# Kernel tuning notes

Measured on AMD Instinct MI355X. Metric: run time of the kernel, lower is better.

The kernel has to match this reference:

```python
import jax, jax.numpy as jnp
import numpy as np

GRID = 3
K = GRID ** 3          # keypoints per proposal (grid rep)
RADIUS = 0.2
NSAMPLE = 16


def _rotz(t):
    c, s = jnp.cos(t), jnp.sin(t)
    z, o = jnp.zeros_like(t), jnp.ones_like(t)
    return jnp.stack([jnp.stack([c, -s, z], -1),
                      jnp.stack([s,  c, z], -1),
                      jnp.stack([z,  z, o], -1)], -2)  # [..., 3, 3]


def _grid_keypoints(boxes, origins, heading):
    # boxes: [B,P,6] = (left,back,down,right,front,up) absolute distances from origin
    B, P, _ = boxes.shape
    ii = jnp.stack(jnp.meshgrid(jnp.arange(GRID), jnp.arange(GRID), jnp.arange(GRID), indexing='ij'), -1)
    dense = ii.reshape(K, 3).astype(boxes.dtype)  # same order as ones(g,g,g).nonzero()
    size = boxes[..., 0:3] + boxes[..., 3:6]                       # [B,P,3]
    local = (dense + 0.5) / GRID * size[:, :, None, :] - boxes[..., None, 0:3]  # [B,P,K,3]
    R = _rotz(heading)                                             # [B,P,3,3]
    pts = jnp.einsum('bpkc,bpcd->bpkd', local, R) + origins[:, :, None, :]
    return pts.reshape(B, P * K, 3)


def _ball_query(key_pts, seed_xyz):
    # key_pts [B,M,3], seed_xyz [B,N,3] -> neighbor indices [B,M,NSAMPLE]
    N = seed_xyz.shape[1]
    d2 = (jnp.sum(key_pts ** 2, -1)[:, :, None]
          + jnp.sum(seed_xyz ** 2, -1)[:, None, :]
          - 2.0 * jnp.einsum('bmc,bnc->bmn', key_pts, seed_xyz))   # [B,M,N]
    cand = jnp.where(d2 < RADIUS ** 2, jnp.arange(N, dtype=jnp.int32), N)
    idx = -jax.lax.top_k(-cand, NSAMPLE)[0]  # first NSAMPLE in-radius indices, ascending
    first = idx[..., 0:1]
    fill = jnp.where(first == N, 0, first)   # empty ball -> index 0 (CUDA kernel default)
    return jnp.where(idx == N, fill, idx)


def _forward(seed_xyz, seed_features, boxes, origins, heading, W1, b1, W2, b2, W3, b3, Wr, br):
    B, P = boxes.shape[:2]
    key_pts = _grid_keypoints(boxes, origins, heading)             # [B,M,3], M=P*K
    idx = _ball_query(key_pts, seed_xyz)                           # [B,M,S]
    b_idx = jnp.arange(B)[:, None, None]
    gx = seed_xyz[b_idx, idx]                                      # [B,M,S,3]
    gf = jnp.transpose(seed_features, (0, 2, 1))[b_idx, idx]       # [B,M,S,C]
    gxyz = (gx - key_pts[:, :, None, :]) / RADIUS                  # normalize_xyz=True
    x = jnp.concatenate([gxyz, gf], -1)                            # use_xyz: [B,M,S,3+C]
    x = jax.nn.relu(x @ W1 + b1)                                   # shared per-point MLP
    x = jax.nn.relu(x @ W2 + b2)
    x = jax.nn.relu(x @ W3 + b3)
    x = jnp.max(x, axis=2)                                         # max-pool over ball -> [B,M,32]
    f = x.reshape(B, P, K, 32)
    # original: [B,32,M] -> view(B,32,P,K) -> transpose(2,3) -> reshape(B,32*K,P)
    f = jnp.transpose(f, (0, 1, 3, 2)).reshape(B, P, 32 * K)       # channel-major (c*K+k) layout
    out = f @ Wr.T + br                                            # 1x1 conv reduce -> [B,P,128]
    return jnp.transpose(out, (0, 2, 1))                           # [B,128,P]


def setup_inputs() -> dict:
    key = jax.random.key(0)
    ks = jax.random.split(key, 9)
    B, N, C, P = 2, 1024, 256, 256
    return {
        'seed_xyz': jax.random.normal(ks[0], (B, N, 3), jnp.float32),
        'seed_features': jax.random.normal(ks[1], (B, C, N), jnp.float32),
        'boxes': jax.random.uniform(ks[2], (B, P, 6), jnp.float32, 0.1, 1.0),
        'origins': jax.random.normal(ks[3], (B, P, 3), jnp.float32),
        'heading': jax.random.uniform(ks[4], (B, P), jnp.float32, 0.0, 6.2831853),
        'W1': jax.random.normal(ks[5], (C + 3, 128), jnp.float32) * 0.05,
        'b1': jnp.zeros((128,), jnp.float32),
        'W2': jax.random.normal(ks[6], (128, 64), jnp.float32) * 0.05,
        'b2': jnp.zeros((64,), jnp.float32),
        'W3': jax.random.normal(ks[7], (64, 32), jnp.float32) * 0.05,
        'b3': jnp.zeros((32,), jnp.float32),
        'Wr': jax.random.normal(ks[8], (128, 32 * K), jnp.float32) * 0.05,
        'br': jnp.zeros((128,), jnp.float32),
    }


def reference(seed_xyz, seed_features, boxes, origins, heading, W1, b1, W2, b2, W3, b3, Wr, br):
    return _forward(seed_xyz, seed_features, boxes, origins, heading, W1, b1, W2, b2, W3, b3, Wr, br)
```

## Files before the change

kernel.cpp:

```cpp
#include <hip/hip_runtime.h>

#define B_ 2
#define N_ 1024
#define C_ 256
#define P_ 256
#define K_ 27
#define M_ (P_ * K_)
#define TOTKP (B_ * M_)
#define NS 16
#define R2C 0.04f
#define QDIM 864


#define PREP_FPRE0   0
#define PREP_WRT0    256
#define PREP_OINIT0  364
#define PREP_BALLQ0  620
#define PREP_NBLK    4076

__global__ __launch_bounds__(256) void prep_k(
    const float* __restrict__ sf, const float* __restrict__ W1,
    const float* __restrict__ b1, const float* __restrict__ Wr,
    const float* __restrict__ br, const float* __restrict__ seed_xyz,
    const float* __restrict__ boxes, const float* __restrict__ origins,
    const float* __restrict__ heading,
    float* __restrict__ F, float* __restrict__ WrT, float* __restrict__ out,
    float4* __restrict__ kp4, int* __restrict__ cntw, int* __restrict__ idxw)
{
    __shared__ __align__(16) float ssf[C_ * 8];
    int tid = threadIdx.x;
    int bid = blockIdx.x;

    if (bid < PREP_WRT0) {
        int b = bid >> 7;
        int n0 = (bid & 127) * 8;
        for (int e = tid; e < C_ * 8; e += 256) {
            int c = e >> 3, i = e & 7;
            ssf[e] = sf[(b * C_ + c) * N_ + n0 + i];
        }
        __syncthreads();
        int j = tid & 127;
        int h = tid >> 7;
        float acc[4];
        float bj = b1[j];
#pragma unroll
        for (int i = 0; i < 4; i++) acc[i] = bj;
#pragma unroll 8
        for (int c = 0; c < C_; ++c) {
            float w = W1[(3 + c) * 128 + j];
            float4 s = *(const float4*)&ssf[c * 8 + h * 4];
            acc[0] = fmaf(s.x, w, acc[0]);
            acc[1] = fmaf(s.y, w, acc[1]);
            acc[2] = fmaf(s.z, w, acc[2]);
            acc[3] = fmaf(s.w, w, acc[3]);
        }
#pragma unroll
        for (int i = 0; i < 4; i++)
            F[(b * N_ + n0 + h * 4 + i) * 128 + j] = acc[i];
    } else if (bid < PREP_OINIT0) {
        int e4 = (bid - PREP_WRT0) * 256 + tid;
        int j = e4 / 216, qq = e4 - j * 216;
        float4 v = ((const float4*)(Wr + j * QDIM))[qq];
        int q0 = qq * 4;
        WrT[(q0 + 0) * 128 + j] = v.x;
        WrT[(q0 + 1) * 128 + j] = v.y;
        WrT[(q0 + 2) * 128 + j] = v.z;
        WrT[(q0 + 3) * 128 + j] = v.w;
    } else if (bid < PREP_BALLQ0) {
        int id = (bid - PREP_OINIT0) * 256 + tid;
        out[id] = br[(id >> 8) & 127];
    } else {
        int wid = tid >> 6, lane = tid & 63;
        int kpg = (bid - PREP_BALLQ0) * 4 + wid;
        int b = kpg / M_;
        int m = kpg - b * M_;
        int p = m / K_, a = m - p * K_;

        const float* bx = boxes + (b * P_ + p) * 6;
        const float* og = origins + (b * P_ + p) * 3;
        float th = heading[b * P_ + p];
        float di = (float)(a / 9), dj = (float)((a / 3) % 3), dk = (float)(a % 3);
        float s0 = __fadd_rn(bx[0], bx[3]);
        float s1 = __fadd_rn(bx[1], bx[4]);
        float s2 = __fadd_rn(bx[2], bx[5]);
        float lx = __fsub_rn(__fmul_rn(__fdiv_rn(__fadd_rn(di, 0.5f), 3.0f), s0), bx[0]);
        float ly = __fsub_rn(__fmul_rn(__fdiv_rn(__fadd_rn(dj, 0.5f), 3.0f), s1), bx[1]);
        float lz = __fsub_rn(__fmul_rn(__fdiv_rn(__fadd_rn(dk, 0.5f), 3.0f), s2), bx[2]);
        float ct = cosf(th), st = sinf(th);
        float kx = __fadd_rn(__fadd_rn(__fmul_rn(lx, ct), __fmul_rn(ly, st)), og[0]);
        float ky = __fadd_rn(__fadd_rn(__fmul_rn(lx, -st), __fmul_rn(ly, ct)), og[1]);
        float kz = __fadd_rn(lz, og[2]);
        if (lane == 0) kp4[kpg] = make_float4(kx, ky, kz, 0.f);
        float kk = __fadd_rn(__fadd_rn(__fmul_rn(kx, kx), __fmul_rn(ky, ky)),
                             __fmul_rn(kz, kz));

        const float* sb = seed_xyz + b * (N_ * 3) + lane * 48;
        float f[48];
#pragma unroll
        for (int q = 0; q < 12; q++)
            ((float4*)f)[q] = ((const float4*)sb)[q];

        unsigned mask = 0;
#pragma unroll
        for (int i = 0; i < 16; i++) {
            float x = f[3 * i], y = f[3 * i + 1], z = f[3 * i + 2];
            float ss = __fadd_rn(__fadd_rn(__fmul_rn(x, x), __fmul_rn(y, y)),
                                 __fmul_rn(z, z));
            float dot = __fadd_rn(__fadd_rn(__fmul_rn(kx, x), __fmul_rn(ky, y)),
                                  __fmul_rn(kz, z));
            float d2 = __fsub_rn(__fadd_rn(kk, ss), __fmul_rn(2.0f, dot));
            mask |= (d2 < R2C ? 1u : 0u) << i;
        }

        int pc = __popc(mask);
        int incl = pc;
#pragma unroll
        for (int d = 1; d < 64; d <<= 1) {
            int v = __shfl_up(incl, d);
            if (lane >= d) incl += v;
        }
        int total = __shfl(incl, 63);
        int base = incl - pc;

        int* ip = idxw + kpg * NS;
        unsigned mm = mask;
        while (mm && base < NS) {
            int i = __ffs(mm) - 1;
            mm &= mm - 1;
            ip[base++] = lane * 16 + i;
        }
        if (lane == 0) cntw[kpg] = total < NS ? total : NS;
    }
}

struct Ctx {
    const float* seed; const float* F;
    const float* sW2; const float* sW3;
    float* sH1; float* sH2;
    const int* ip;
    float4 kp;
    float w1x0, w1y0, w1z0, w1x1, w1y1, w1z1, b2j, b3t;
    int lane, t, jh, b, cnt, n0;
};

template <int GS>
static __device__ __forceinline__ void do_group(const Ctx& c, int s0, float& pool)
{
    float gx[GS], gy[GS], gz[GS];
    int nn[GS];
#pragma unroll
    for (int u = 0; u < GS; u++) {
        int s = s0 + u;
        int n = (s < c.cnt) ? c.ip[s] : c.n0;
        nn[u] = n;
        const float* sp = c.seed + (c.b * N_ + n) * 3;
        gx[u] = __fdiv_rn(__fsub_rn(sp[0], c.kp.x), 0.2f);
        gy[u] = __fdiv_rn(__fsub_rn(sp[1], c.kp.y), 0.2f);
        gz[u] = __fdiv_rn(__fsub_rn(sp[2], c.kp.z), 0.2f);
    }
#pragma unroll
    for (int u = 0; u < GS; u++) {
        const float* fp = c.F + (c.b * N_ + nn[u]) * 128;
        float v0 = fp[c.lane];
        float v1 = fp[c.lane + 64];
        v0 = fmaf(gx[u], c.w1x0, fmaf(gy[u], c.w1y0, fmaf(gz[u], c.w1z0, v0)));
        v1 = fmaf(gx[u], c.w1x1, fmaf(gy[u], c.w1y1, fmaf(gz[u], c.w1z1, v1)));
        c.sH1[u * 128 + c.lane] = fmaxf(v0, 0.f);
        c.sH1[u * 128 + c.lane + 64] = fmaxf(v1, 0.f);
    }
    float acc[GS];
#pragma unroll
    for (int u = 0; u < GS; u++) acc[u] = c.b2j;
#pragma unroll
    for (int cc = 0; cc < 128; cc += 4) {
        float w0 = c.sW2[(cc + 0) * 64 + c.lane];
        float w1 = c.sW2[(cc + 1) * 64 + c.lane];
        float w2 = c.sW2[(cc + 2) * 64 + c.lane];
        float w3 = c.sW2[(cc + 3) * 64 + c.lane];
#pragma unroll
        for (int u = 0; u < GS; u++) {
            float4 h = *(const float4*)&c.sH1[u * 128 + cc];
            acc[u] = fmaf(h.x, w0, fmaf(h.y, w1, fmaf(h.z, w2, fmaf(h.w, w3, acc[u]))));
        }
    }
#pragma unroll
    for (int u = 0; u < GS; u++) c.sH2[u * 64 + c.lane] = fmaxf(acc[u], 0.f);
    float a3[GS];
#pragma unroll
    for (int u = 0; u < GS; u++) a3[u] = (c.jh == 0) ? c.b3t : 0.f;
#pragma unroll
    for (int jj = 0; jj < 32; jj += 4) {
        int j0 = c.jh * 32 + jj;
        float w0 = c.sW3[(j0 + 0) * 32 + c.t];
        float w1 = c.sW3[(j0 + 1) * 32 + c.t];
        float w2 = c.sW3[(j0 + 2) * 32 + c.t];
        float w3 = c.sW3[(j0 + 3) * 32 + c.t];
#pragma unroll
        for (int u = 0; u < GS; u++) {
            float4 h = *(const float4*)&c.sH2[u * 64 + j0];
            a3[u] = fmaf(h.x, w0, fmaf(h.y, w1, fmaf(h.z, w2, fmaf(h.w, w3, a3[u]))));
        }
    }
#pragma unroll
    for (int u = 0; u < GS; u++) {
        float v = a3[u] + __shfl_xor(a3[u], 32);
        pool = fmaxf(pool, fmaxf(v, 0.f));
    }
}

__global__ __launch_bounds__(256) void pool_k(
    const float* __restrict__ seed_xyz, const float* __restrict__ F,
    const float* __restrict__ W1, const float* __restrict__ b2g,
    const float* __restrict__ b3g, const float* __restrict__ W2g,
    const float* __restrict__ W3g, const float4* __restrict__ kp4,
    const int* __restrict__ cntw, const int* __restrict__ idxw,
    float* __restrict__ pooled)
{
    __shared__ __align__(16) float sW2[128 * 64];
    __shared__ __align__(16) float sW3[64 * 32];
    __shared__ __align__(16) float sH1[4 * 4 * 128];
    __shared__ __align__(16) float sH2[4 * 4 * 64];
    int tid = threadIdx.x;
    for (int e = tid; e < 2048; e += 256)
        ((float4*)sW2)[e] = ((const float4*)W2g)[e];
    for (int e = tid; e < 512; e += 256)
        ((float4*)sW3)[e] = ((const float4*)W3g)[e];
    __syncthreads();

    int wid = tid >> 6, lane = tid & 63;
    Ctx c;
    c.seed = seed_xyz; c.F = F;
    c.sW2 = sW2; c.sW3 = sW3;
    c.sH1 = sH1 + wid * 4 * 128;
    c.sH2 = sH2 + wid * 4 * 64;
    c.lane = lane; c.t = lane & 31; c.jh = lane >> 5;
    c.w1x0 = W1[lane];       c.w1x1 = W1[lane + 64];
    c.w1y0 = W1[128 + lane]; c.w1y1 = W1[128 + lane + 64];
    c.w1z0 = W1[256 + lane]; c.w1z1 = W1[256 + lane + 64];
    c.b2j = b2g[lane]; c.b3t = b3g[lane & 31];

    for (int i = 0; i < 2; ++i) {
        int kpg = blockIdx.x * 8 + wid * 2 + i;
        c.kp = kp4[kpg];
        c.cnt = cntw[kpg];
        c.ip = idxw + kpg * NS;
        c.b = kpg / M_;
        c.n0 = (c.cnt > 0) ? c.ip[0] : 0;
        int scnt = c.cnt < 1 ? 1 : c.cnt;
        float pool = 0.f;
        for (int s0 = 0; s0 < scnt; s0 += 4) {
            int gs = scnt - s0; gs = gs > 4 ? 4 : gs;
            switch (gs) {
                case 1: do_group<1>(c, s0, pool); break;
                case 2: do_group<2>(c, s0, pool); break;
                case 3: do_group<3>(c, s0, pool); break;
                default: do_group<4>(c, s0, pool); break;
            }
        }
        if (lane < 32) pooled[kpg * 32 + lane] = pool;
    }
}

__global__ __launch_bounds__(256) void final_k(
    const float* __restrict__ pooled, const float* __restrict__ WrT,
    float* __restrict__ out)
{
    __shared__ __align__(16) float ft[8][108];
    int tid = threadIdx.x;
    int blk = blockIdx.x;
    int c = blk & 7;
    int mt = blk >> 3;
    if (tid < 216) {
        int ri = tid / 27, k = tid - ri * 27;
        int row = mt * 8 + ri;
        int b = row >> 8, p = row & 255;
        const float* sp = pooled + ((b * M_ + p * K_) + k) * 32 + c * 4;
        float4 v = *(const float4*)sp;
        float* fp = &ft[ri][0];
        fp[k] = v.x; fp[27 + k] = v.y; fp[54 + k] = v.z; fp[81 + k] = v.w;
    }
    __syncthreads();
    int j = tid & 127;
    int rh = tid >> 7;
    float a0 = 0.f, a1 = 0.f, a2 = 0.f, a3 = 0.f;
    const float* wp = WrT + (c * 108) * 128 + j;
    const float* f0 = &ft[rh * 4 + 0][0];
    const float* f1 = &ft[rh * 4 + 1][0];
    const float* f2 = &ft[rh * 4 + 2][0];
    const float* f3 = &ft[rh * 4 + 3][0];
#pragma unroll 4
    for (int q = 0; q < 108; ++q) {
        float w = wp[q * 128];
        a0 = fmaf(f0[q], w, a0);
        a1 = fmaf(f1[q], w, a1);
        a2 = fmaf(f2[q], w, a2);
        a3 = fmaf(f3[q], w, a3);
    }
    int row0 = mt * 8 + rh * 4;
    int b0 = row0 >> 8;
    int p0 = row0 & 255;
    float* op = out + b0 * 128 * 256 + j * 256 + p0;
    atomicAdd(op + 0, a0);
    atomicAdd(op + 1, a1);
    atomicAdd(op + 2, a2);
    atomicAdd(op + 3, a3);
}

extern "C" void kernel_launch(void* const* d_in, const int* in_sizes, int n_in,
                              void* d_out, int out_size, void* d_ws, size_t ws_size,
                              hipStream_t stream)
{
    const float* seed_xyz  = (const float*)d_in[0];
    const float* seed_feat = (const float*)d_in[1];
    const float* boxes     = (const float*)d_in[2];
    const float* origins   = (const float*)d_in[3];
    const float* heading   = (const float*)d_in[4];
    const float* W1        = (const float*)d_in[5];
    const float* b1        = (const float*)d_in[6];
    const float* W2        = (const float*)d_in[7];
    const float* b2        = (const float*)d_in[8];
    const float* W3        = (const float*)d_in[9];
    const float* b3        = (const float*)d_in[10];
    const float* Wr        = (const float*)d_in[11];
    const float* br        = (const float*)d_in[12];
    float* out = (float*)d_out;

    char* ws = (char*)d_ws;
    float4* kp4    = (float4*)(ws);
    int*    cntw   = (int*)(ws + 221184);
    int*    idxw   = (int*)(ws + 276480);
    float*  F      = (float*)(ws + 1161216);
    float*  pooled = (float*)(ws + 2209792);
    float*  WrT    = (float*)(ws + 3979264);

    prep_k<<<dim3(PREP_NBLK), dim3(256), 0, stream>>>(
        seed_feat, W1, b1, Wr, br, seed_xyz, boxes, origins, heading,
        F, WrT, out, kp4, cntw, idxw);
    pool_k<<<dim3(1728), dim3(256), 0, stream>>>(seed_xyz, F, W1, b2, b3, W2, W3,
                                                 kp4, cntw, idxw, pooled);
    final_k<<<dim3(512), dim3(256), 0, stream>>>(pooled, WrT, out);
}
```

Before: 162.0 us.

## Fuse pooling and final projection into one per-proposal kernel

Merges pool_k and final_k into a single kernel where each block handles one proposal: its 27 keypoints are pooled into shared memory, then the proposal's 864-wide feature is multiplied by WrT in place. This drops the pooled intermediate buffer, one kernel launch, the output-initialization blocks and the atomic adds, and the bias is now added directly. In exchange the grid shrinks from 1728 to 512 blocks, and the 27 keypoints are spread unevenly over 4 waves, which may reduce parallelism and load balance.

```diff
diff --git a/kernel.cpp b/kernel.cpp
--- a/kernel.cpp
+++ b/kernel.cpp
@@ -12,19 +12,16 @@
 #define QDIM 864
 
 
-#define PREP_FPRE0   0
 #define PREP_WRT0    256
-#define PREP_OINIT0  364
-#define PREP_BALLQ0  620
-#define PREP_NBLK    4076
+#define PREP_BALLQ0  364
+#define PREP_NBLK    3820
 
 __global__ __launch_bounds__(256) void prep_k(
     const float* __restrict__ sf, const float* __restrict__ W1,
     const float* __restrict__ b1, const float* __restrict__ Wr,
-    const float* __restrict__ br, const float* __restrict__ seed_xyz,
-    const float* __restrict__ boxes, const float* __restrict__ origins,
-    const float* __restrict__ heading,
-    float* __restrict__ F, float* __restrict__ WrT, float* __restrict__ out,
+    const float* __restrict__ seed_xyz, const float* __restrict__ boxes,
+    const float* __restrict__ origins, const float* __restrict__ heading,
+    float* __restrict__ F, float* __restrict__ WrT,
     float4* __restrict__ kp4, int* __restrict__ cntw, int* __restrict__ idxw)
 {
     __shared__ __align__(16) float ssf[C_ * 8];
@@ -57,7 +54,7 @@
 #pragma unroll
         for (int i = 0; i < 4; i++)
             F[(b * N_ + n0 + h * 4 + i) * 128 + j] = acc[i];
-    } else if (bid < PREP_OINIT0) {
+    } else if (bid < PREP_BALLQ0) {
         int e4 = (bid - PREP_WRT0) * 256 + tid;
         int j = e4 / 216, qq = e4 - j * 216;
         float4 v = ((const float4*)(Wr + j * QDIM))[qq];
@@ -66,9 +63,6 @@
         WrT[(q0 + 1) * 128 + j] = v.y;
         WrT[(q0 + 2) * 128 + j] = v.z;
         WrT[(q0 + 3) * 128 + j] = v.w;
-    } else if (bid < PREP_BALLQ0) {
-        int id = (bid - PREP_OINIT0) * 256 + tid;
-        out[id] = br[(id >> 8) & 127];
     } else {
         int wid = tid >> 6, lane = tid & 63;
         int kpg = (bid - PREP_BALLQ0) * 4 + wid;
@@ -208,43 +202,49 @@
     }
 }
 
-__global__ __launch_bounds__(256) void pool_k(
+__global__ __launch_bounds__(256, 2) void pf_k(
     const float* __restrict__ seed_xyz, const float* __restrict__ F,
     const float* __restrict__ W1, const float* __restrict__ b2g,
     const float* __restrict__ b3g, const float* __restrict__ W2g,
-    const float* __restrict__ W3g, const float4* __restrict__ kp4,
+    const float* __restrict__ W3g, const float* __restrict__ WrT,
+    const float* __restrict__ br, const float4* __restrict__ kp4,
     const int* __restrict__ cntw, const int* __restrict__ idxw,
-    float* __restrict__ pooled)
+    float* __restrict__ out)
 {
     __shared__ __align__(16) float sW2[128 * 64];
     __shared__ __align__(16) float sW3[64 * 32];
     __shared__ __align__(16) float sH1[4 * 4 * 128];
     __shared__ __align__(16) float sH2[4 * 4 * 64];
+    __shared__ __align__(16) float ft[QDIM];
+    __shared__ __align__(16) float pj[128];
     int tid = threadIdx.x;
     for (int e = tid; e < 2048; e += 256)
         ((float4*)sW2)[e] = ((const float4*)W2g)[e];
     for (int e = tid; e < 512; e += 256)
         ((float4*)sW3)[e] = ((const float4*)W3g)[e];
-    __syncthreads();
 
     int wid = tid >> 6, lane = tid & 63;
+    int bp = blockIdx.x;
+    int b = bp >> 8, p = bp & 255;
+
     Ctx c;
     c.seed = seed_xyz; c.F = F;
     c.sW2 = sW2; c.sW3 = sW3;
     c.sH1 = sH1 + wid * 4 * 128;
     c.sH2 = sH2 + wid * 4 * 64;
     c.lane = lane; c.t = lane & 31; c.jh = lane >> 5;
+    c.b = b;
     c.w1x0 = W1[lane];       c.w1x1 = W1[lane + 64];
     c.w1y0 = W1[128 + lane]; c.w1y1 = W1[128 + lane + 64];
     c.w1z0 = W1[256 + lane]; c.w1z1 = W1[256 + lane + 64];
     c.b2j = b2g[lane]; c.b3t = b3g[lane & 31];
-
-    for (int i = 0; i < 2; ++i) {
-        int kpg = blockIdx.x * 8 + wid * 2 + i;
+    __syncthreads();
+
+    for (int k = wid; k < K_; k += 4) {
+        int kpg = bp * K_ + k;
         c.kp = kp4[kpg];
         c.cnt = cntw[kpg];
         c.ip = idxw + kpg * NS;
-        c.b = kpg / M_;
         c.n0 = (c.cnt > 0) ? c.ip[0] : 0;
         int scnt = c.cnt < 1 ? 1 : c.cnt;
         float pool = 0.f;
@@ -257,53 +257,22 @@
                 default: do_group<4>(c, s0, pool); break;
             }
         }
-        if (lane < 32) pooled[kpg * 32 + lane] = pool;
-    }
-}
-
-__global__ __launch_bounds__(256) void final_k(
-    const float* __restrict__ pooled, const float* __restrict__ WrT,
-    float* __restrict__ out)
-{
-    __shared__ __align__(16) float ft[8][108];
-    int tid = threadIdx.x;
-    int blk = blockIdx.x;
-    int c = blk & 7;
-    int mt = blk >> 3;
-    if (tid < 216) {
-        int ri = tid / 27, k = tid - ri * 27;
-        int row = mt * 8 + ri;
-        int b = row >> 8, p = row & 255;
-        const float* sp = pooled + ((b * M_ + p * K_) + k) * 32 + c * 4;
-        float4 v = *(const float4*)sp;
-        float* fp = &ft[ri][0];
-        fp[k] = v.x; fp[27 + k] = v.y; fp[54 + k] = v.z; fp[81 + k] = v.w;
+        if (lane < 32) ft[lane * K_ + k] = pool;
     }
     __syncthreads();
+
     int j = tid & 127;
-    int rh = tid >> 7;
-    float a0 = 0.f, a1 = 0.f, a2 = 0.f, a3 = 0.f;
-    const float* wp = WrT + (c * 108) * 128 + j;
-    const float* f0 = &ft[rh * 4 + 0][0];
-    const float* f1 = &ft[rh * 4 + 1][0];
-    const float* f2 = &ft[rh * 4 + 2][0];
-    const float* f3 = &ft[rh * 4 + 3][0];
+    int h = tid >> 7;
+    float a = 0.f;
+    const float* fq = ft + h * 432;
+    const float* wq = WrT + (h * 432) * 128 + j;
 #pragma unroll 4
-    for (int q = 0; q < 108; ++q) {
-        float w = wp[q * 128];
-        a0 = fmaf(f0[q], w, a0);
-        a1 = fmaf(f1[q], w, a1);
-        a2 = fmaf(f2[q], w, a2);
-        a3 = fmaf(f3[q], w, a3);
-    }
-    int row0 = mt * 8 + rh * 4;
-    int b0 = row0 >> 8;
-    int p0 = row0 & 255;
-    float* op = out + b0 * 128 * 256 + j * 256 + p0;
-    atomicAdd(op + 0, a0);
-    atomicAdd(op + 1, a1);
-    atomicAdd(op + 2, a2);
-    atomicAdd(op + 3, a3);
+    for (int q = 0; q < 432; ++q)
+        a = fmaf(fq[q], wq[q * 128], a);
+    if (h == 1) pj[j] = a;
+    __syncthreads();
+    if (h == 0)
+        out[(b * 128 + j) * 256 + p] = a + pj[j] + br[j];
 }
 
 extern "C" void kernel_launch(void* const* d_in, const int* in_sizes, int n_in,
@@ -326,17 +295,15 @@
     float* out = (float*)d_out;
 
     char* ws = (char*)d_ws;
-    float4* kp4    = (float4*)(ws);
-    int*    cntw   = (int*)(ws + 221184);
-    int*    idxw   = (int*)(ws + 276480);
-    float*  F      = (float*)(ws + 1161216);
-    float*  pooled = (float*)(ws + 2209792);
-    float*  WrT    = (float*)(ws + 3979264);
+    float4* kp4  = (float4*)(ws);
+    int*    cntw = (int*)(ws + 221184);
+    int*    idxw = (int*)(ws + 276480);
+    float*  F    = (float*)(ws + 1161216);
+    float*  WrT  = (float*)(ws + 2209792);
 
     prep_k<<<dim3(PREP_NBLK), dim3(256), 0, stream>>>(
-        seed_feat, W1, b1, Wr, br, seed_xyz, boxes, origins, heading,
-        F, WrT, out, kp4, cntw, idxw);
-    pool_k<<<dim3(1728), dim3(256), 0, stream>>>(seed_xyz, F, W1, b2, b3, W2, W3,
-                                                 kp4, cntw, idxw, pooled);
-    final_k<<<dim3(512), dim3(256), 0, stream>>>(pooled, WrT, out);
+        seed_feat, W1, b1, Wr, seed_xyz, boxes, origins, heading,
+        F, WrT, kp4, cntw, idxw);
+    pf_k<<<dim3(512), dim3(256), 0, stream>>>(
+        seed_xyz, F, W1, b2, b3, W2, W3, WrT, br, kp4, cntw, idxw, out);
 }
```

Result: faster. 148.5 us (-8.3%).
